# Kernel optimization log

Hardware: AMD Instinct MI355X
Metric: run time of the kernel (lower is better)

The kernel has to match this reference:

```python
import jax, jax.numpy as jnp
import numpy as np

N_ATOMS = 50000
N_PAIRS = 1600000
N_BASIS = 128
N_FILTERS = 128
N_RBF = 20
LOG2 = float(np.log(2.0))


def ssp(x):
    # ShiftedSoftplus: softplus(x) - log(2)
    return jax.nn.softplus(x) - LOG2


def setup_inputs() -> dict:
    key = jax.random.key(0)
    ks = jax.random.split(key, 16)

    def lin(k, fan_in, fan_out):
        bound = 1.0 / np.sqrt(fan_in)
        kw, kb = jax.random.split(k)
        W = jax.random.uniform(kw, (fan_in, fan_out), jnp.float32, -bound, bound)
        b = jax.random.uniform(kb, (fan_out,), jnp.float32, -bound, bound)
        return W, b

    W_in, b_in = lin(ks[0], N_BASIS, N_FILTERS)
    Wf1, bf1 = lin(ks[1], N_RBF, N_FILTERS)
    Wf2, bf2 = lin(ks[2], N_FILTERS, N_FILTERS)
    Wo1, bo1 = lin(ks[3], N_FILTERS, N_BASIS)
    Wo2, bo2 = lin(ks[4], N_BASIS, N_BASIS)

    return {
        "x": jax.random.normal(ks[5], (N_ATOMS, N_BASIS), jnp.float32),
        "f_ij": jax.random.uniform(ks[6], (N_PAIRS, N_RBF), jnp.float32),
        "rcut_ij": jax.random.uniform(ks[7], (N_PAIRS,), jnp.float32),
        "W_in": W_in, "b_in": b_in,
        "Wf1": Wf1, "bf1": bf1, "Wf2": Wf2, "bf2": bf2,
        "Wo1": Wo1, "bo1": bo1, "Wo2": Wo2, "bo2": bo2,
        "idx_i": jax.random.randint(ks[8], (N_PAIRS,), 0, N_ATOMS, jnp.int32),
        "idx_j": jax.random.randint(ks[9], (N_PAIRS,), 0, N_ATOMS, jnp.int32),
    }


def reference(x, f_ij, rcut_ij, W_in, b_in, Wf1, bf1, Wf2, bf2, Wo1, bo1, Wo2, bo2, idx_i, idx_j):
    # input_to_feature
    h = x @ W_in + b_in                                  # [N, F]
    # filter network: Linear -> ssp -> Linear, then cutoff scaling
    Wij = ssp(f_ij @ Wf1 + bf1) @ Wf2 + bf2              # [E, F]
    Wij = Wij * rcut_ij[:, None]
    # gather - multiply - scatter_add
    x_ij = h[idx_j] * Wij                                # [E, F]
    agg = jax.ops.segment_sum(x_ij, idx_i, num_segments=h.shape[0])  # [N, F]
    # feature_to_output: Linear -> ssp -> Linear
    out = ssp(agg @ Wo1 + bo1) @ Wo2 + bo2               # [N, B]
    return out
```

## Files before the change

kernel.cpp:

```cpp
#include <hip/hip_runtime.h>
#include <math.h>

#define N_ATOMS 50000
#define N_PAIRS 1600000
#define NF 128
#define NRBF 20
#define NTILES (N_PAIRS / 64)

typedef _Float16 half8 __attribute__((ext_vector_type(8)));
typedef float floatx4 __attribute__((ext_vector_type(4)));

__device__ __forceinline__ float sspf(float x) {
    float t = __expf(-fabsf(x));
    return fmaxf(x, 0.0f) + __logf(1.0f + t) - 0.69314718055994530942f;
}

__device__ __forceinline__ int swz16(int row, int k8) {
    return row * 256 + ((k8 ^ (row & 15)) << 4);
}

template<int NTHR>
__device__ __forceinline__ void stage_w(const float* __restrict__ W, char* dst, int t) {
    for (int i = t; i < 128 * 128; i += NTHR) {
        int c = i & 127, k = i >> 7;
        *(_Float16*)(dst + swz16(c, k >> 3) + ((k & 7) << 1)) = (_Float16)W[k * 128 + c];
    }
}

template<typename TIN, typename TOUT, bool SSP_OUT, bool ZERO>
__global__ __launch_bounds__(256) void gemm_mfma_kernel(
    const TIN* __restrict__ A, const float* __restrict__ W,
    const float* __restrict__ bias, TOUT* __restrict__ out, int M,
    float* __restrict__ zbuf, int zcount4)
{
    __shared__ char sW[32768];
    const int t = threadIdx.x;
    const int w = t >> 6, lane = t & 63, m = lane & 15, q = lane >> 4;

    if (ZERO) {
        float4 z = {0.f, 0.f, 0.f, 0.f};
        for (int i = blockIdx.x * 256 + t; i < zcount4; i += gridDim.x * 256)
            ((float4*)zbuf)[i] = z;
    }
    stage_w<256>(W, sW, t);
    float bv[8];
    #pragma unroll
    for (int g = 0; g < 8; ++g) bv[g] = bias[g * 16 + m];
    __syncthreads();

    const floatx4 zero4 = {0.f, 0.f, 0.f, 0.f};
    const int ntiles = (M + 63) >> 6;
    for (int tile = blockIdx.x; tile < ntiles; tile += gridDim.x) {
        const int arow = tile * 64 + w * 16 + m;
        half8 a[4];
        if (arow < M) {
            const TIN* ap = A + (size_t)arow * 128;
            #pragma unroll
            for (int s = 0; s < 4; ++s) {
                if (sizeof(TIN) == 2) {
                    a[s] = *(const half8*)(ap + s * 32 + q * 8);
                } else {
                    float4 u0 = *(const float4*)((const float*)ap + s * 32 + q * 8);
                    float4 u1 = *(const float4*)((const float*)ap + s * 32 + q * 8 + 4);
                    a[s][0] = (_Float16)u0.x; a[s][1] = (_Float16)u0.y;
                    a[s][2] = (_Float16)u0.z; a[s][3] = (_Float16)u0.w;
                    a[s][4] = (_Float16)u1.x; a[s][5] = (_Float16)u1.y;
                    a[s][6] = (_Float16)u1.z; a[s][7] = (_Float16)u1.w;
                }
            }
        } else {
            #pragma unroll
            for (int s = 0; s < 4; ++s) a[s] = (half8){};
        }
        floatx4 acc[8];
        #pragma unroll
        for (int g = 0; g < 8; ++g) {
            floatx4 c = zero4;
            #pragma unroll
            for (int s = 0; s < 4; ++s) {
                half8 b = *(const half8*)(sW + swz16(g * 16 + m, 4 * s + q));
                c = __builtin_amdgcn_mfma_f32_16x16x32_f16(a[s], b, c, 0, 0, 0);
            }
            acc[g] = c;
        }
        #pragma unroll
        for (int r = 0; r < 4; ++r) {
            const int grow = tile * 64 + w * 16 + q * 4 + r;
            if (grow < M) {
                TOUT* op = out + (size_t)grow * 128;
                #pragma unroll
                for (int g = 0; g < 8; ++g) {
                    float v = acc[g][r] + bv[g];
                    if (SSP_OUT) v = sspf(v);
                    op[g * 16 + m] = (TOUT)v;
                }
            }
        }
    }
}

__global__ __launch_bounds__(256) void edge_kernel(
    const float* __restrict__ f_ij, const float* __restrict__ rcut,
    const float* __restrict__ Wf1, const float* __restrict__ bf1,
    const float* __restrict__ Wf2, const float* __restrict__ bf2,
    const int* __restrict__ idx_i, const int* __restrict__ idx_j,
    const _Float16* __restrict__ h, float* __restrict__ agg)
{
    __shared__ char sW2[32768];
    __shared__ char sS[4][4096];
    const int t = threadIdx.x;
    const int w = t >> 6, lane = t & 63, m = lane & 15, q = lane >> 4;

    stage_w<256>(Wf2, sW2, t);
    half8 bW1[8];
    #pragma unroll
    for (int g = 0; g < 8; ++g) {
        #pragma unroll
        for (int j = 0; j < 8; ++j) {
            int k = q * 8 + j;
            bW1[g][j] = (k < NRBF) ? (_Float16)Wf1[k * 128 + g * 16 + m] : (_Float16)0.0f;
        }
    }
    float bf1r[8], bf2r[8];
    #pragma unroll
    for (int g = 0; g < 8; ++g) { bf1r[g] = bf1[g * 16 + m]; bf2r[g] = bf2[g * 16 + m]; }
    __syncthreads();

    char* mySS = sS[w];
    const floatx4 zero4 = {0.f, 0.f, 0.f, 0.f};
    const float4 fz = {0.f, 0.f, 0.f, 0.f};
    const int stride = gridDim.x;

    float4 f0 = fz, f1 = fz; int4 jj4;
    {
        int e0 = blockIdx.x * 64 + w * 16;
        const float* fb = f_ij + (size_t)(e0 + m) * NRBF + q * 8;
        if (q < 2)      { f0 = *(const float4*)fb; f1 = *(const float4*)(fb + 4); }
        else if (q == 2){ f0 = *(const float4*)fb; }
        jj4 = *(const int4*)&idx_j[e0 + q * 4];
    }

    for (int tile = blockIdx.x; tile < NTILES; tile += stride) {
        const int e0 = tile * 64 + w * 16;
        int ntile = tile + stride; if (ntile >= NTILES) ntile = tile;

        int jj[4] = {jj4.x, jj4.y, jj4.z, jj4.w};
        _Float16 hv[4][8];
        #pragma unroll
        for (int r = 0; r < 4; ++r) {
            const _Float16* hp = h + (size_t)jj[r] * 128;
            #pragma unroll
            for (int g = 0; g < 8; ++g) hv[r][g] = hp[g * 16 + m];
        }
        int4 ii4 = *(const int4*)&idx_i[e0 + q * 4];
        float4 rc4 = *(const float4*)&rcut[e0 + q * 4];

        half8 a1;
        a1[0]=(_Float16)f0.x; a1[1]=(_Float16)f0.y; a1[2]=(_Float16)f0.z; a1[3]=(_Float16)f0.w;
        a1[4]=(_Float16)f1.x; a1[5]=(_Float16)f1.y; a1[6]=(_Float16)f1.z; a1[7]=(_Float16)f1.w;
        floatx4 c1[8];
        #pragma unroll
        for (int g = 0; g < 8; ++g)
            c1[g] = __builtin_amdgcn_mfma_f32_16x16x32_f16(a1, bW1[g], zero4, 0, 0, 0);

        float4 nf0 = fz, nf1 = fz; int4 njj4;
        {
            int ne0 = ntile * 64 + w * 16;
            const float* fb = f_ij + (size_t)(ne0 + m) * NRBF + q * 8;
            if (q < 2)      { nf0 = *(const float4*)fb; nf1 = *(const float4*)(fb + 4); }
            else if (q == 2){ nf0 = *(const float4*)fb; }
            njj4 = *(const int4*)&idx_j[ne0 + q * 4];
        }

        #pragma unroll
        for (int g = 0; g < 8; ++g) {
            #pragma unroll
            for (int r = 0; r < 4; ++r) {
                float v = sspf(c1[g][r] + bf1r[g]);
                *(_Float16*)(mySS + swz16(q * 4 + r, 2 * g + (m >> 3)) + ((m & 7) << 1)) =
                    (_Float16)v;
            }
        }

        half8 a2[4];
        #pragma unroll
        for (int s = 0; s < 4; ++s)
            a2[s] = *(const half8*)(mySS + swz16(m, 4 * s + q));

        floatx4 acc[8];
        #pragma unroll
        for (int g = 0; g < 8; ++g) {
            floatx4 c = zero4;
            #pragma unroll
            for (int s = 0; s < 4; ++s) {
                half8 b = *(const half8*)(sW2 + swz16(g * 16 + m, 4 * s + q));
                c = __builtin_amdgcn_mfma_f32_16x16x32_f16(a2[s], b, c, 0, 0, 0);
            }
            acc[g] = c;
        }

        int ii[4] = {ii4.x, ii4.y, ii4.z, ii4.w};
        float rc[4] = {rc4.x, rc4.y, rc4.z, rc4.w};
        #pragma unroll
        for (int r = 0; r < 4; ++r) {
            float* arow = agg + (size_t)ii[r] * 128;
            #pragma unroll
            for (int g = 0; g < 8; ++g) {
                float wij = (acc[g][r] + bf2r[g]) * rc[r];
                atomicAdd(&arow[g * 16 + m], (float)hv[r][g] * wij);
            }
        }

        f0 = nf0; f1 = nf1; jj4 = njj4;
    }
}

extern "C" void kernel_launch(void* const* d_in, const int* in_sizes, int n_in,
                              void* d_out, int out_size, void* d_ws, size_t ws_size,
                              hipStream_t stream) {
    const float* x     = (const float*)d_in[0];
    const float* f_ij  = (const float*)d_in[1];
    const float* rcutp = (const float*)d_in[2];
    const float* W_in  = (const float*)d_in[3];
    const float* b_in  = (const float*)d_in[4];
    const float* Wf1   = (const float*)d_in[5];
    const float* bf1   = (const float*)d_in[6];
    const float* Wf2   = (const float*)d_in[7];
    const float* bf2   = (const float*)d_in[8];
    const float* Wo1   = (const float*)d_in[9];
    const float* bo1   = (const float*)d_in[10];
    const float* Wo2   = (const float*)d_in[11];
    const float* bo2   = (const float*)d_in[12];
    const int* idx_i   = (const int*)d_in[13];
    const int* idx_j   = (const int*)d_in[14];
    float* out = (float*)d_out;

    float*     agg = (float*)d_ws;
    _Float16*  h   = (_Float16*)((char*)d_ws + (size_t)N_ATOMS * NF * 4);
    _Float16*  tmp = h;

    const int zc4 = N_ATOMS * NF / 4;
    gemm_mfma_kernel<float, _Float16, false, true>
        <<<dim3(782), 256, 0, stream>>>(x, W_in, b_in, h, N_ATOMS, agg, zc4);
    edge_kernel<<<dim3(768), 256, 0, stream>>>(f_ij, rcutp, Wf1, bf1, Wf2, bf2,
                                               idx_i, idx_j, h, agg);
    gemm_mfma_kernel<float, _Float16, true, false>
        <<<dim3(782), 256, 0, stream>>>(agg, Wo1, bo1, tmp, N_ATOMS, nullptr, 0);
    gemm_mfma_kernel<_Float16, float, false, false>
        <<<dim3(782), 256, 0, stream>>>(tmp, Wo2, bo2, out, N_ATOMS, nullptr, 0);
}
```

Measured before the change: 916.7 us.

## Replace edge atomics with CSR segment reduction over destination atoms

Builds a CSR layout of edges sorted by destination atom (histogram, single-block scan, atomic scatter). The edge kernel then assigns one wavefront per atom and reduces its edges in registers, writing each agg row once instead of issuing float atomics per edge element. Weight matrices are converted once into swizzled fp16 images by a prep kernel so that GEMM blocks only copy them. The cost is three extra passes over idx_i, a serial single-block scan, irregular gathers of f_ij and rcut through the edge permutation, and partial 16-edge tiles that waste MFMA work on atoms with few edges.

```diff
diff --git a/kernel.cpp b/kernel.cpp
--- a/kernel.cpp
+++ b/kernel.cpp
@@ -5,7 +5,6 @@
 #define N_PAIRS 1600000
 #define NF 128
 #define NRBF 20
-#define NTILES (N_PAIRS / 64)
 
 typedef _Float16 half8 __attribute__((ext_vector_type(8)));
 typedef float floatx4 __attribute__((ext_vector_type(4)));
@@ -19,30 +18,83 @@
     return row * 256 + ((k8 ^ (row & 15)) << 4);
 }
 
+__global__ __launch_bounds__(256) void prep_kernel(
+    const float* __restrict__ W_in, const float* __restrict__ Wf2,
+    const float* __restrict__ Wo1, const float* __restrict__ Wo2,
+    _Float16* __restrict__ Wimg, int* __restrict__ woffs)
+{
+    const int b = blockIdx.x;
+    const float* W = (b == 0) ? W_in : (b == 1) ? Wf2 : (b == 2) ? Wo1 : Wo2;
+    char* img = (char*)(Wimg + b * 16384);
+    for (int i = threadIdx.x; i < 16384; i += 256) {
+        int c = i & 127, k = i >> 7;
+        *(_Float16*)(img + swz16(c, k >> 3) + ((k & 7) << 1)) = (_Float16)W[k * 128 + c];
+    }
+    for (int i = b * 256 + threadIdx.x; i < N_ATOMS; i += 1024) woffs[i] = 0;
+}
+
+__global__ __launch_bounds__(256) void hist_kernel(
+    const int* __restrict__ idx_i, int* __restrict__ cnt)
+{
+    for (int e = blockIdx.x * 256 + threadIdx.x; e < N_PAIRS; e += gridDim.x * 256)
+        atomicAdd(&cnt[idx_i[e]], 1);
+}
+
+__global__ __launch_bounds__(1024) void scan_kernel(
+    int* __restrict__ woffs, int* __restrict__ offs)
+{
+    __shared__ int sc[1024];
+    const int t = threadIdx.x;
+    const int CH = 49;
+    int lo = t * CH, hi = lo + CH;
+    if (lo > N_ATOMS) lo = N_ATOMS;
+    if (hi > N_ATOMS) hi = N_ATOMS;
+    int s = 0;
+    for (int i = lo; i < hi; ++i) s += woffs[i];
+    sc[t] = s;
+    __syncthreads();
+    for (int off = 1; off < 1024; off <<= 1) {
+        int v = (t >= off) ? sc[t - off] : 0;
+        __syncthreads();
+        sc[t] += v;
+        __syncthreads();
+    }
+    int run = sc[t] - s;
+    for (int i = lo; i < hi; ++i) {
+        int c = woffs[i];
+        offs[i] = run;
+        woffs[i] = run;
+        run += c;
+    }
+    if (hi == N_ATOMS && lo < N_ATOMS) offs[N_ATOMS] = run;
+}
+
+__global__ __launch_bounds__(256) void scatter_kernel(
+    const int* __restrict__ idx_i, int* __restrict__ woffs, int* __restrict__ eid_s)
+{
+    for (int e = blockIdx.x * 256 + threadIdx.x; e < N_PAIRS; e += gridDim.x * 256) {
+        int pos = atomicAdd(&woffs[idx_i[e]], 1);
+        eid_s[pos] = e;
+    }
+}
+
 template<int NTHR>
-__device__ __forceinline__ void stage_w(const float* __restrict__ W, char* dst, int t) {
-    for (int i = t; i < 128 * 128; i += NTHR) {
-        int c = i & 127, k = i >> 7;
-        *(_Float16*)(dst + swz16(c, k >> 3) + ((k & 7) << 1)) = (_Float16)W[k * 128 + c];
-    }
-}
-
-template<typename TIN, typename TOUT, bool SSP_OUT, bool ZERO>
+__device__ __forceinline__ void stage_img(const _Float16* __restrict__ img, char* dst, int t) {
+    const float4* s = (const float4*)img;
+    float4* d = (float4*)dst;
+    for (int i = t; i < 2048; i += NTHR) d[i] = s[i];
+}
+
+template<typename TIN, typename TOUT, bool SSP_OUT>
 __global__ __launch_bounds__(256) void gemm_mfma_kernel(
-    const TIN* __restrict__ A, const float* __restrict__ W,
-    const float* __restrict__ bias, TOUT* __restrict__ out, int M,
-    float* __restrict__ zbuf, int zcount4)
+    const TIN* __restrict__ A, const _Float16* __restrict__ Wimg,
+    const float* __restrict__ bias, TOUT* __restrict__ out, int M)
 {
     __shared__ char sW[32768];
     const int t = threadIdx.x;
     const int w = t >> 6, lane = t & 63, m = lane & 15, q = lane >> 4;
 
-    if (ZERO) {
-        float4 z = {0.f, 0.f, 0.f, 0.f};
-        for (int i = blockIdx.x * 256 + t; i < zcount4; i += gridDim.x * 256)
-            ((float4*)zbuf)[i] = z;
-    }
-    stage_w<256>(W, sW, t);
+    stage_img<256>(Wimg, sW, t);
     float bv[8];
     #pragma unroll
     for (int g = 0; g < 8; ++g) bv[g] = bias[g * 16 + m];
@@ -99,11 +151,12 @@
     }
 }
 
-__global__ __launch_bounds__(256) void edge_kernel(
+__global__ __launch_bounds__(256, 3) void edge_kernel(
     const float* __restrict__ f_ij, const float* __restrict__ rcut,
     const float* __restrict__ Wf1, const float* __restrict__ bf1,
-    const float* __restrict__ Wf2, const float* __restrict__ bf2,
-    const int* __restrict__ idx_i, const int* __restrict__ idx_j,
+    const _Float16* __restrict__ Wf2img, const float* __restrict__ bf2,
+    const int* __restrict__ idx_j,
+    const int* __restrict__ offs, const int* __restrict__ eid_s,
     const _Float16* __restrict__ h, float* __restrict__ agg)
 {
     __shared__ char sW2[32768];
@@ -111,7 +164,7 @@
     const int t = threadIdx.x;
     const int w = t >> 6, lane = t & 63, m = lane & 15, q = lane >> 4;
 
-    stage_w<256>(Wf2, sW2, t);
+    stage_img<256>(Wf2img, sW2, t);
     half8 bW1[8];
     #pragma unroll
     for (int g = 0; g < 8; ++g) {
@@ -129,89 +182,87 @@
     char* mySS = sS[w];
     const floatx4 zero4 = {0.f, 0.f, 0.f, 0.f};
     const float4 fz = {0.f, 0.f, 0.f, 0.f};
-    const int stride = gridDim.x;
-
-    float4 f0 = fz, f1 = fz; int4 jj4;
-    {
-        int e0 = blockIdx.x * 64 + w * 16;
-        const float* fb = f_ij + (size_t)(e0 + m) * NRBF + q * 8;
-        if (q < 2)      { f0 = *(const float4*)fb; f1 = *(const float4*)(fb + 4); }
-        else if (q == 2){ f0 = *(const float4*)fb; }
-        jj4 = *(const int4*)&idx_j[e0 + q * 4];
-    }
-
-    for (int tile = blockIdx.x; tile < NTILES; tile += stride) {
-        const int e0 = tile * 64 + w * 16;
-        int ntile = tile + stride; if (ntile >= NTILES) ntile = tile;
-
-        int jj[4] = {jj4.x, jj4.y, jj4.z, jj4.w};
-        _Float16 hv[4][8];
-        #pragma unroll
-        for (int r = 0; r < 4; ++r) {
-            const _Float16* hp = h + (size_t)jj[r] * 128;
-            #pragma unroll
-            for (int g = 0; g < 8; ++g) hv[r][g] = hp[g * 16 + m];
-        }
-        int4 ii4 = *(const int4*)&idx_i[e0 + q * 4];
-        float4 rc4 = *(const float4*)&rcut[e0 + q * 4];
-
-        half8 a1;
-        a1[0]=(_Float16)f0.x; a1[1]=(_Float16)f0.y; a1[2]=(_Float16)f0.z; a1[3]=(_Float16)f0.w;
-        a1[4]=(_Float16)f1.x; a1[5]=(_Float16)f1.y; a1[6]=(_Float16)f1.z; a1[7]=(_Float16)f1.w;
-        floatx4 c1[8];
-        #pragma unroll
-        for (int g = 0; g < 8; ++g)
-            c1[g] = __builtin_amdgcn_mfma_f32_16x16x32_f16(a1, bW1[g], zero4, 0, 0, 0);
-
-        float4 nf0 = fz, nf1 = fz; int4 njj4;
-        {
-            int ne0 = ntile * 64 + w * 16;
-            const float* fb = f_ij + (size_t)(ne0 + m) * NRBF + q * 8;
-            if (q < 2)      { nf0 = *(const float4*)fb; nf1 = *(const float4*)(fb + 4); }
-            else if (q == 2){ nf0 = *(const float4*)fb; }
-            njj4 = *(const int4*)&idx_j[ne0 + q * 4];
+    const int wid = blockIdx.x * 4 + w;
+    const int nw = gridDim.x * 4;
+
+    for (int a = wid; a < N_ATOMS; a += nw) {
+        const int start = offs[a], end = offs[a + 1];
+        float racc[8];
+        #pragma unroll
+        for (int g = 0; g < 8; ++g) racc[g] = 0.f;
+
+        for (int base = start; base < end; base += 16) {
+            int em = base + m; if (em >= end) em = end - 1;
+            const int eidm = eid_s[em];
+            const float* fb = f_ij + (size_t)eidm * NRBF + q * 8;
+            float4 f0 = fz, f1 = fz;
+            if (q < 2)       { f0 = *(const float4*)fb; f1 = *(const float4*)(fb + 4); }
+            else if (q == 2) { f0 = *(const float4*)fb; }
+
+            int jj[4]; float rc[4];
+            #pragma unroll
+            for (int r = 0; r < 4; ++r) {
+                int s = base + q * 4 + r;
+                int vs = (s < end) ? s : end - 1;
+                int e = eid_s[vs];
+                jj[r] = idx_j[e];
+                rc[r] = (s < end) ? rcut[e] : 0.f;
+            }
+
+            _Float16 hv[4][8];
+            #pragma unroll
+            for (int r = 0; r < 4; ++r) {
+                const _Float16* hp = h + (size_t)jj[r] * NF;
+                #pragma unroll
+                for (int g = 0; g < 8; ++g) hv[r][g] = hp[g * 16 + m];
+            }
+
+            half8 a1;
+            a1[0] = (_Float16)f0.x; a1[1] = (_Float16)f0.y;
+            a1[2] = (_Float16)f0.z; a1[3] = (_Float16)f0.w;
+            a1[4] = (_Float16)f1.x; a1[5] = (_Float16)f1.y;
+            a1[6] = (_Float16)f1.z; a1[7] = (_Float16)f1.w;
+            floatx4 c1[8];
+            #pragma unroll
+            for (int g = 0; g < 8; ++g)
+                c1[g] = __builtin_amdgcn_mfma_f32_16x16x32_f16(a1, bW1[g], zero4, 0, 0, 0);
+
+            #pragma unroll
+            for (int g = 0; g < 8; ++g) {
+                #pragma unroll
+                for (int r = 0; r < 4; ++r) {
+                    float v = sspf(c1[g][r] + bf1r[g]);
+                    *(_Float16*)(mySS + swz16(q * 4 + r, 2 * g + (m >> 3)) + ((m & 7) << 1)) =
+                        (_Float16)v;
+                }
+            }
+
+            half8 a2[4];
+            #pragma unroll
+            for (int s = 0; s < 4; ++s)
+                a2[s] = *(const half8*)(mySS + swz16(m, 4 * s + q));
+
+            #pragma unroll
+            for (int g = 0; g < 8; ++g) {
+                floatx4 c = zero4;
+                #pragma unroll
+                for (int s = 0; s < 4; ++s) {
+                    half8 b = *(const half8*)(sW2 + swz16(g * 16 + m, 4 * s + q));
+                    c = __builtin_amdgcn_mfma_f32_16x16x32_f16(a2[s], b, c, 0, 0, 0);
+                }
+                #pragma unroll
+                for (int r = 0; r < 4; ++r)
+                    racc[g] += ((c[r] + bf2r[g]) * rc[r]) * (float)hv[r][g];
+            }
         }
 
         #pragma unroll
         for (int g = 0; g < 8; ++g) {
-            #pragma unroll
-            for (int r = 0; r < 4; ++r) {
-                float v = sspf(c1[g][r] + bf1r[g]);
-                *(_Float16*)(mySS + swz16(q * 4 + r, 2 * g + (m >> 3)) + ((m & 7) << 1)) =
-                    (_Float16)v;
-            }
-        }
-
-        half8 a2[4];
-        #pragma unroll
-        for (int s = 0; s < 4; ++s)
-            a2[s] = *(const half8*)(mySS + swz16(m, 4 * s + q));
-
-        floatx4 acc[8];
-        #pragma unroll
-        for (int g = 0; g < 8; ++g) {
-            floatx4 c = zero4;
-            #pragma unroll
-            for (int s = 0; s < 4; ++s) {
-                half8 b = *(const half8*)(sW2 + swz16(g * 16 + m, 4 * s + q));
-                c = __builtin_amdgcn_mfma_f32_16x16x32_f16(a2[s], b, c, 0, 0, 0);
-            }
-            acc[g] = c;
-        }
-
-        int ii[4] = {ii4.x, ii4.y, ii4.z, ii4.w};
-        float rc[4] = {rc4.x, rc4.y, rc4.z, rc4.w};
-        #pragma unroll
-        for (int r = 0; r < 4; ++r) {
-            float* arow = agg + (size_t)ii[r] * 128;
-            #pragma unroll
-            for (int g = 0; g < 8; ++g) {
-                float wij = (acc[g][r] + bf2r[g]) * rc[r];
-                atomicAdd(&arow[g * 16 + m], (float)hv[r][g] * wij);
-            }
-        }
-
-        f0 = nf0; f1 = nf1; jj4 = njj4;
+            float v = racc[g];
+            v += __shfl_xor(v, 16, 64);
+            v += __shfl_xor(v, 32, 64);
+            if (q == 0) agg[(size_t)a * NF + g * 16 + m] = v;
+        }
     }
 }
 
@@ -235,17 +286,25 @@
     const int* idx_j   = (const int*)d_in[14];
     float* out = (float*)d_out;
 
-    float*     agg = (float*)d_ws;
-    _Float16*  h   = (_Float16*)((char*)d_ws + (size_t)N_ATOMS * NF * 4);
-    _Float16*  tmp = h;
-
-    const int zc4 = N_ATOMS * NF / 4;
-    gemm_mfma_kernel<float, _Float16, false, true>
-        <<<dim3(782), 256, 0, stream>>>(x, W_in, b_in, h, N_ATOMS, agg, zc4);
-    edge_kernel<<<dim3(768), 256, 0, stream>>>(f_ij, rcutp, Wf1, bf1, Wf2, bf2,
-                                               idx_i, idx_j, h, agg);
-    gemm_mfma_kernel<float, _Float16, true, false>
-        <<<dim3(782), 256, 0, stream>>>(agg, Wo1, bo1, tmp, N_ATOMS, nullptr, 0);
-    gemm_mfma_kernel<_Float16, float, false, false>
-        <<<dim3(782), 256, 0, stream>>>(tmp, Wo2, bo2, out, N_ATOMS, nullptr, 0);
-}
+    char* ws = (char*)d_ws;
+    float*    agg   = (float*)ws;
+    _Float16* h     = (_Float16*)(ws + 25600000);
+    int*      eid_s = (int*)(ws + 38400000);
+    int*      offs  = (int*)(ws + 44800000);
+    int*      woffs = (int*)(ws + 45000016);
+    _Float16* Wimg  = (_Float16*)(ws + 45200016);
+    _Float16* tmp   = h;
+
+    prep_kernel<<<dim3(4), 256, 0, stream>>>(W_in, Wf2, Wo1, Wo2, Wimg, woffs);
+    gemm_mfma_kernel<float, _Float16, false>
+        <<<dim3(782), 256, 0, stream>>>(x, Wimg, b_in, h, N_ATOMS);
+    hist_kernel<<<dim3(1024), 256, 0, stream>>>(idx_i, woffs);
+    scan_kernel<<<dim3(1), 1024, 0, stream>>>(woffs, offs);
+    scatter_kernel<<<dim3(1024), 256, 0, stream>>>(idx_i, woffs, eid_s);
+    edge_kernel<<<dim3(768), 256, 0, stream>>>(f_ij, rcutp, Wf1, bf1, Wimg + 16384, bf2,
+                                               idx_j, offs, eid_s, h, agg);
+    gemm_mfma_kernel<float, _Float16, true>
+        <<<dim3(782), 256, 0, stream>>>(agg, Wimg + 32768, bo1, tmp, N_ATOMS);
+    gemm_mfma_kernel<_Float16, float, false>
+        <<<dim3(782), 256, 0, stream>>>(tmp, Wimg + 49152, bo2, out, N_ATOMS);
+}
```

Result: slower. 1.826 ms (+99.2%).

## Counting-sort edges by destination atom and reduce in registers before atomics

Applied to the files above, without the earlier changes.

Adds a histogram, a single-block scan and a scatter pass that bucket edges by idx_i into padded 16-edge tiles. The f_ij rows are stored as fp16 and idx_j as u16. The edge kernel walks contiguous tile ranges per wave, accumulates each atom's contributions in registers, and issues one atomicAdd per atom segment instead of one per edge feature. Weight matrices are converted to a swizzled fp16 image once in a prep kernel, so the GEMM blocks no longer convert them per block. The trade-off is extra passes over the edge data, a serial-ish single-block scan, padding waste in the MFMA tiles, and a large workspace requirement; if the workspace is too small, it falls back to the old atomic kernel.

```diff
diff --git a/kernel.cpp b/kernel.cpp
--- a/kernel.cpp
+++ b/kernel.cpp
@@ -5,10 +5,13 @@
 #define N_PAIRS 1600000
 #define NF 128
 #define NRBF 20
-#define NTILES (N_PAIRS / 64)
+#define PADCAP 2200000
+#define NTILE_CAP (PADCAP / 16)
 
 typedef _Float16 half8 __attribute__((ext_vector_type(8)));
 typedef float floatx4 __attribute__((ext_vector_type(4)));
+typedef unsigned long long u64;
+typedef unsigned short u16;
 
 __device__ __forceinline__ float sspf(float x) {
     float t = __expf(-fabsf(x));
@@ -19,17 +22,96 @@
     return row * 256 + ((k8 ^ (row & 15)) << 4);
 }
 
+__global__ __launch_bounds__(256) void prep_kernel(
+    const float* __restrict__ W_in, const float* __restrict__ Wf2,
+    const float* __restrict__ Wo1, const float* __restrict__ Wo2,
+    _Float16* __restrict__ Wimg, int* __restrict__ woffs)
+{
+    const int b = blockIdx.x;
+    const float* W = (b == 0) ? W_in : (b == 1) ? Wf2 : (b == 2) ? Wo1 : Wo2;
+    char* img = (char*)(Wimg + b * 16384);
+    for (int i = threadIdx.x; i < 16384; i += 256) {
+        int c = i & 127, k = i >> 7;
+        *(_Float16*)(img + swz16(c, k >> 3) + ((k & 7) << 1)) = (_Float16)W[k * 128 + c];
+    }
+    for (int i = b * 256 + threadIdx.x; i < N_ATOMS; i += 1024) woffs[i] = 0;
+}
+
+__global__ __launch_bounds__(256) void hist_kernel(
+    const int* __restrict__ idx_i, int* __restrict__ cnt)
+{
+    for (int e = blockIdx.x * 256 + threadIdx.x; e < N_PAIRS; e += gridDim.x * 256)
+        atomicAdd(&cnt[idx_i[e]], 1);
+}
+
+__global__ __launch_bounds__(1024) void scan_kernel(
+    int* __restrict__ woffs, int* __restrict__ desc, int* __restrict__ meta)
+{
+    __shared__ int sc[1024];
+    const int t = threadIdx.x;
+    const int CH = 49;
+    int lo = t * CH, hi = lo + CH;
+    if (lo > N_ATOMS) lo = N_ATOMS;
+    if (hi > N_ATOMS) hi = N_ATOMS;
+    int s = 0;
+    for (int i = lo; i < hi; ++i) s += (woffs[i] + 15) >> 4;
+    sc[t] = s;
+    __syncthreads();
+    for (int off = 1; off < 1024; off <<= 1) {
+        int v = (t >= off) ? sc[t - off] : 0;
+        __syncthreads();
+        sc[t] += v;
+        __syncthreads();
+    }
+    int tb = sc[t] - s;
+    for (int i = lo; i < hi; ++i) {
+        int c = woffs[i];
+        int nt = (c + 15) >> 4;
+        woffs[i] = tb * 16;
+        for (int k = 0; k < nt; ++k) {
+            int nv = c - k * 16; if (nv > 16) nv = 16;
+            if (tb + k < NTILE_CAP) desc[tb + k] = (i << 5) | nv;
+        }
+        tb += nt;
+    }
+    if (t == 1023) { int NT = sc[1023]; meta[0] = NT < NTILE_CAP ? NT : NTILE_CAP; }
+}
+
+__global__ __launch_bounds__(256) void scatter_permute_kernel(
+    const float* __restrict__ f_ij, const float* __restrict__ rcut,
+    const int* __restrict__ idx_i, const int* __restrict__ idx_j,
+    int* __restrict__ woffs, u16* __restrict__ f_s,
+    float* __restrict__ rc_s, u16* __restrict__ j_s)
+{
+    for (int e = blockIdx.x * 256 + threadIdx.x; e < N_PAIRS; e += gridDim.x * 256) {
+        int pos = atomicAdd(&woffs[idx_i[e]], 1);
+        if (pos >= PADCAP) continue;
+        const float4* fr = (const float4*)(f_ij + (size_t)e * NRBF);
+        u16* dst = f_s + (size_t)pos * 20;
+        #pragma unroll
+        for (int v = 0; v < 5; ++v) {
+            float4 fv = fr[v];
+            union { _Float16 hf; u16 b; } c0, c1, c2, c3;
+            c0.hf = (_Float16)fv.x; c1.hf = (_Float16)fv.y;
+            c2.hf = (_Float16)fv.z; c3.hf = (_Float16)fv.w;
+            ushort4 o; o.x = c0.b; o.y = c1.b; o.z = c2.b; o.w = c3.b;
+            *(ushort4*)(dst + v * 4) = o;
+        }
+        rc_s[pos] = rcut[e];
+        j_s[pos] = (u16)idx_j[e];
+    }
+}
+
 template<int NTHR>
-__device__ __forceinline__ void stage_w(const float* __restrict__ W, char* dst, int t) {
-    for (int i = t; i < 128 * 128; i += NTHR) {
-        int c = i & 127, k = i >> 7;
-        *(_Float16*)(dst + swz16(c, k >> 3) + ((k & 7) << 1)) = (_Float16)W[k * 128 + c];
-    }
+__device__ __forceinline__ void stage_img(const _Float16* __restrict__ img, char* dst, int t) {
+    const float4* s = (const float4*)img;
+    float4* d = (float4*)dst;
+    for (int i = t; i < 2048; i += NTHR) d[i] = s[i];
 }
 
 template<typename TIN, typename TOUT, bool SSP_OUT, bool ZERO>
 __global__ __launch_bounds__(256) void gemm_mfma_kernel(
-    const TIN* __restrict__ A, const float* __restrict__ W,
+    const TIN* __restrict__ A, const _Float16* __restrict__ Wimg,
     const float* __restrict__ bias, TOUT* __restrict__ out, int M,
     float* __restrict__ zbuf, int zcount4)
 {
@@ -42,7 +124,7 @@
         for (int i = blockIdx.x * 256 + t; i < zcount4; i += gridDim.x * 256)
             ((float4*)zbuf)[i] = z;
     }
-    stage_w<256>(W, sW, t);
+    stage_img<256>(Wimg, sW, t);
     float bv[8];
     #pragma unroll
     for (int g = 0; g < 8; ++g) bv[g] = bias[g * 16 + m];
@@ -100,10 +182,11 @@
 }
 
 __global__ __launch_bounds__(256) void edge_kernel(
-    const float* __restrict__ f_ij, const float* __restrict__ rcut,
+    const u64* __restrict__ f_s, const float* __restrict__ rc_s,
+    const u16* __restrict__ j_s, const int* __restrict__ desc,
+    const int* __restrict__ meta,
     const float* __restrict__ Wf1, const float* __restrict__ bf1,
-    const float* __restrict__ Wf2, const float* __restrict__ bf2,
-    const int* __restrict__ idx_i, const int* __restrict__ idx_j,
+    const _Float16* __restrict__ Wf2img, const float* __restrict__ bf2,
     const _Float16* __restrict__ h, float* __restrict__ agg)
 {
     __shared__ char sW2[32768];
@@ -111,7 +194,142 @@
     const int t = threadIdx.x;
     const int w = t >> 6, lane = t & 63, m = lane & 15, q = lane >> 4;
 
-    stage_w<256>(Wf2, sW2, t);
+    stage_img<256>(Wf2img, sW2, t);
+    half8 bW1[8];
+    #pragma unroll
+    for (int g = 0; g < 8; ++g) {
+        #pragma unroll
+        for (int j = 0; j < 8; ++j) {
+            int k = q * 8 + j;
+            bW1[g][j] = (k < NRBF) ? (_Float16)Wf1[k * 128 + g * 16 + m] : (_Float16)0.0f;
+        }
+    }
+    float bf1r[8], bf2r[8];
+    #pragma unroll
+    for (int g = 0; g < 8; ++g) { bf1r[g] = bf1[g * 16 + m]; bf2r[g] = bf2[g * 16 + m]; }
+    __syncthreads();
+
+    char* mySS = sS[w];
+    const floatx4 zero4 = {0.f, 0.f, 0.f, 0.f};
+    const int NT = meta[0];
+    const int nw = gridDim.x * 4;
+    const int wid = blockIdx.x * 4 + w;
+    const int T = (NT + nw - 1) / nw;
+    int t0 = wid * T, t1 = t0 + T;
+    if (t1 > NT) t1 = NT;
+    if (t0 >= t1) return;
+
+    auto loadtile = [&](int tt, int& d_, u64& x0_, u64& x1_, int* jjv, float4& rcv) {
+        d_ = desc[tt];
+        const u64* fr = f_s + (size_t)(tt * 16 + m) * 5;
+        u64 x0 = 0, x1 = 0;
+        if (q < 2)       { x0 = fr[2 * q]; x1 = fr[2 * q + 1]; }
+        else if (q == 2) { x0 = fr[4]; }
+        x0_ = x0; x1_ = x1;
+        ushort4 jv = *(const ushort4*)(j_s + tt * 16 + q * 4);
+        jjv[0] = jv.x; jjv[1] = jv.y; jjv[2] = jv.z; jjv[3] = jv.w;
+        rcv = *(const float4*)(rc_s + tt * 16 + q * 4);
+    };
+
+    int d; u64 u0, u1; int jj[4]; float4 rc4;
+    loadtile(t0, d, u0, u1, jj, rc4);
+
+    float racc[8];
+    #pragma unroll
+    for (int g = 0; g < 8; ++g) racc[g] = 0.f;
+
+    for (int tt = t0; tt < t1; ++tt) {
+        const int nv = d & 31;
+        const int atom = d >> 5;
+
+        float rcarr[4] = {rc4.x, rc4.y, rc4.z, rc4.w};
+        float rc[4]; int jm[4];
+        #pragma unroll
+        for (int r = 0; r < 4; ++r) {
+            int sidx = q * 4 + r;
+            bool ok = sidx < nv;
+            jm[r] = ok ? jj[r] : 0;
+            rc[r] = ok ? rcarr[r] : 0.f;
+        }
+        _Float16 hv[4][8];
+        #pragma unroll
+        for (int r = 0; r < 4; ++r) {
+            const _Float16* hp = h + (size_t)jm[r] * NF;
+            #pragma unroll
+            for (int g = 0; g < 8; ++g) hv[r][g] = hp[g * 16 + m];
+        }
+        int nd = 0; u64 nu0 = 0, nu1 = 0; int njj[4] = {0, 0, 0, 0};
+        float4 nrc4 = {0.f, 0.f, 0.f, 0.f};
+        if (tt + 1 < t1) loadtile(tt + 1, nd, nu0, nu1, njj, nrc4);
+
+        union { u64 u[2]; half8 v; } cv;
+        cv.u[0] = u0; cv.u[1] = u1;
+        half8 a1 = cv.v;
+        if (m >= nv) a1 = (half8){};
+
+        floatx4 c1[8];
+        #pragma unroll
+        for (int g = 0; g < 8; ++g)
+            c1[g] = __builtin_amdgcn_mfma_f32_16x16x32_f16(a1, bW1[g], zero4, 0, 0, 0);
+
+        #pragma unroll
+        for (int g = 0; g < 8; ++g) {
+            #pragma unroll
+            for (int r = 0; r < 4; ++r) {
+                float v = sspf(c1[g][r] + bf1r[g]);
+                *(_Float16*)(mySS + swz16(q * 4 + r, 2 * g + (m >> 3)) + ((m & 7) << 1)) =
+                    (_Float16)v;
+            }
+        }
+        half8 a2[4];
+        #pragma unroll
+        for (int s = 0; s < 4; ++s)
+            a2[s] = *(const half8*)(mySS + swz16(m, 4 * s + q));
+
+        #pragma unroll
+        for (int g = 0; g < 8; ++g) {
+            floatx4 c = zero4;
+            #pragma unroll
+            for (int s = 0; s < 4; ++s) {
+                half8 b = *(const half8*)(sW2 + swz16(g * 16 + m, 4 * s + q));
+                c = __builtin_amdgcn_mfma_f32_16x16x32_f16(a2[s], b, c, 0, 0, 0);
+            }
+            #pragma unroll
+            for (int r = 0; r < 4; ++r)
+                racc[g] += ((c[r] + bf2r[g]) * rc[r]) * (float)hv[r][g];
+        }
+
+        bool last = (tt + 1 >= t1);
+        if (last || (nd >> 5) != atom) {
+            #pragma unroll
+            for (int g = 0; g < 8; ++g) {
+                float v = racc[g];
+                v += __shfl_xor(v, 16, 64);
+                v += __shfl_xor(v, 32, 64);
+                if (q == 0) atomicAdd(&agg[(size_t)atom * NF + g * 16 + m], v);
+                racc[g] = 0.f;
+            }
+        }
+        d = nd; u0 = nu0; u1 = nu1;
+        jj[0] = njj[0]; jj[1] = njj[1]; jj[2] = njj[2]; jj[3] = njj[3];
+        rc4 = nrc4;
+    }
+}
+
+__global__ __launch_bounds__(256) void edge_atomic_kernel(
+    const float* __restrict__ f_ij, const float* __restrict__ rcut,
+    const float* __restrict__ Wf1, const float* __restrict__ bf1,
+    const _Float16* __restrict__ Wf2img, const float* __restrict__ bf2,
+    const int* __restrict__ idx_i, const int* __restrict__ idx_j,
+    const _Float16* __restrict__ h, float* __restrict__ agg)
+{
+    __shared__ char sW2[32768];
+    __shared__ char sS[4][4096];
+    const int NTILES = N_PAIRS / 64;
+    const int t = threadIdx.x;
+    const int w = t >> 6, lane = t & 63, m = lane & 15, q = lane >> 4;
+
+    stage_img<256>(Wf2img, sW2, t);
     half8 bW1[8];
     #pragma unroll
     for (int g = 0; g < 8; ++g) {
@@ -181,7 +399,6 @@
                     (_Float16)v;
             }
         }
-
         half8 a2[4];
         #pragma unroll
         for (int s = 0; s < 4; ++s)
@@ -210,7 +427,6 @@
                 atomicAdd(&arow[g * 16 + m], (float)hv[r][g] * wij);
             }
         }
-
         f0 = nf0; f1 = nf1; jj4 = njj4;
     }
 }
@@ -235,17 +451,39 @@
     const int* idx_j   = (const int*)d_in[14];
     float* out = (float*)d_out;
 
-    float*     agg = (float*)d_ws;
-    _Float16*  h   = (_Float16*)((char*)d_ws + (size_t)N_ATOMS * NF * 4);
-    _Float16*  tmp = h;
+    char* ws = (char*)d_ws;
+    float*     agg   = (float*)ws;
+    _Float16*  h     = (_Float16*)(ws + 25600000);
+    _Float16*  Wimg  = (_Float16*)(ws + 38400000);
+    int*       woffs = (int*)(ws + 38531072);
+    int*       meta  = (int*)(ws + 38731072);
+    int*       desc  = (int*)(ws + 38731088);
+    float*     rc_s  = (float*)(ws + 39281104);
+    u16*       j_s   = (u16*)(ws + 48081104);
+    u16*       f_s   = (u16*)(ws + 52481104);
+    _Float16*  tmp   = h;
+    const size_t NEED = 140481104;
 
     const int zc4 = N_ATOMS * NF / 4;
+    prep_kernel<<<dim3(4), 256, 0, stream>>>(W_in, Wf2, Wo1, Wo2, Wimg, woffs);
     gemm_mfma_kernel<float, _Float16, false, true>
-        <<<dim3(782), 256, 0, stream>>>(x, W_in, b_in, h, N_ATOMS, agg, zc4);
-    edge_kernel<<<dim3(768), 256, 0, stream>>>(f_ij, rcutp, Wf1, bf1, Wf2, bf2,
-                                               idx_i, idx_j, h, agg);
+        <<<dim3(782), 256, 0, stream>>>(x, Wimg, b_in, h, N_ATOMS, agg, zc4);
+
+    if (ws_size >= NEED) {
+        hist_kernel<<<dim3(1024), 256, 0, stream>>>(idx_i, woffs);
+        scan_kernel<<<dim3(1), 1024, 0, stream>>>(woffs, desc, meta);
+        scatter_permute_kernel<<<dim3(1024), 256, 0, stream>>>(
+            f_ij, rcutp, idx_i, idx_j, woffs, f_s, rc_s, j_s);
+        edge_kernel<<<dim3(768), 256, 0, stream>>>(
+            (const u64*)f_s, rc_s, j_s, desc, meta,
+            Wf1, bf1, Wimg + 16384, bf2, h, agg);
+    } else {
+        edge_atomic_kernel<<<dim3(768), 256, 0, stream>>>(
+            f_ij, rcutp, Wf1, bf1, Wimg + 16384, bf2, idx_i, idx_j, h, agg);
+    }
+
     gemm_mfma_kernel<float, _Float16, true, false>
-        <<<dim3(782), 256, 0, stream>>>(agg, Wo1, bo1, tmp, N_ATOMS, nullptr, 0);
+        <<<dim3(782), 256, 0, stream>>>(agg, Wimg + 32768, bo1, tmp, N_ATOMS, nullptr, 0);
     gemm_mfma_kernel<_Float16, float, false, false>
-        <<<dim3(782), 256, 0, stream>>>(tmp, Wo2, bo2, out, N_ATOMS, nullptr, 0);
-}
+        <<<dim3(782), 256, 0, stream>>>(tmp, Wimg + 49152, bo2, out, N_ATOMS, nullptr, 0);
+}
```

After: 913.7 us. About the same (-0.3%).
